# Kernel optimization log

Hardware: AMD Instinct MI355X
Metric: run time of the kernel (lower is better)

The kernel has to match this reference:

```python
import jax, jax.numpy as jnp
import numpy as np

D_MODEL = 1024
N_HEADS = 16
D_HEAD = D_MODEL // N_HEADS
B, T = 2, 2048
EPS = 1e-5


def setup_inputs() -> dict:
    key = jax.random.key(0)
    ks = jax.random.split(key, 5)
    s = 1.0 / np.sqrt(D_MODEL)
    return {
        "x": jax.random.normal(ks[0], (B, T, D_MODEL), dtype=jnp.float32),
        "W_q": jax.random.normal(ks[1], (D_MODEL, D_MODEL), dtype=jnp.float32) * s,
        "W_k": jax.random.normal(ks[2], (D_MODEL, D_MODEL), dtype=jnp.float32) * s,
        "W_v": jax.random.normal(ks[3], (D_MODEL, D_MODEL), dtype=jnp.float32) * s,
        "W_o": jax.random.normal(ks[4], (D_MODEL, D_MODEL), dtype=jnp.float32) * s,
        "gn_weight": jnp.ones((D_MODEL,), dtype=jnp.float32),
        "gn_bias": jnp.zeros((D_MODEL,), dtype=jnp.float32),
    }


def reference(x, W_q, W_k, W_v, W_o, gn_weight, gn_bias):
    b, t, dm = x.shape
    h, dh = N_HEADS, D_HEAD
    # per-head decay factors gamma_i = 1 - 2^(-5-i)
    gammas = 1.0 - 2.0 ** (-5.0 - jnp.arange(h, dtype=jnp.float32))  # [H]

    # projections (torch Linear: y = x @ W.T), split heads -> [B,T,H,Dh]
    q = (x @ W_q.T).reshape(b, t, h, dh)
    k = (x @ W_k.T).reshape(b, t, h, dh)
    v = (x @ W_v.T).reshape(b, t, h, dh)

    # causal decay mask D[h,i,j] = gamma_h^(i-j) for i>=j else 0
    idx = jnp.arange(t)
    diff = idx[:, None] - idx[None, :]                      # [T,T]
    pow_ = jnp.maximum(diff, 0).astype(jnp.float32)
    decay = jnp.where(diff >= 0, gammas[:, None, None] ** pow_, 0.0)  # [H,T,T]

    scale = jnp.sqrt(jnp.float32(dh))
    attn = jnp.einsum('bihd,bjhd->bhij', q, k) * decay[None] / scale  # [B,H,T,T]
    y = jnp.einsum('bhij,bjhd->bihd', attn, v)               # [B,T,H,Dh]

    # GroupNorm(n_heads, d_model) over channels-first layout: per (b, head)
    # normalize over (T, d_head)
    mean = y.mean(axis=(1, 3), keepdims=True)
    var = y.var(axis=(1, 3), keepdims=True)
    yn = (y - mean) / jnp.sqrt(var + EPS)
    yn = yn.reshape(b, t, dm) * gn_weight + gn_bias

    return yn @ W_o.T
```

## Files before the change

kernel.cpp:

```cpp
#include <hip/hip_runtime.h>
#include <stdint.h>


#define SEQ 2048

typedef __bf16 bf16x8 __attribute__((ext_vector_type(8)));
typedef float  floatx4 __attribute__((ext_vector_type(4)));
typedef unsigned short ushort4v __attribute__((ext_vector_type(4)));

__device__ __forceinline__ unsigned short f2bf(float f){
    __bf16 h = (__bf16)f;
    return __builtin_bit_cast(unsigned short, h);
}

__device__ __forceinline__ void gload_lds16(const void* g, void* l){
    __builtin_amdgcn_global_load_lds(
        (const __attribute__((address_space(1))) unsigned int*)g,
        (__attribute__((address_space(3))) unsigned int*)l, 16, 0, 0);
}

__global__ __launch_bounds__(256)
void cvt_all(const float* __restrict__ x,
             const float* __restrict__ w0, const float* __restrict__ w1,
             const float* __restrict__ w2, const float* __restrict__ w3,
             unsigned short* __restrict__ xb,
             unsigned short* __restrict__ o0, unsigned short* __restrict__ o1,
             unsigned short* __restrict__ o2, unsigned short* __restrict__ o3,
             float* __restrict__ st){
    const int blk = blockIdx.x;
    if(blk == 0 && threadIdx.x < 128) st[threadIdx.x] = 0.0f;
    const float* src; unsigned short* dst; size_t i;
    if(blk < 4096){ src = x; dst = xb; i = (size_t)blk*256 + threadIdx.x; }
    else {
        const int seg = (blk - 4096) >> 10;
        src = seg==0?w0:seg==1?w1:seg==2?w2:w3;
        dst = seg==0?o0:seg==1?o1:seg==2?o2:o3;
        i = (size_t)((blk - 4096) & 1023)*256 + threadIdx.x;
    }
    float4 v = ((const float4*)src)[i];
    ushort4v o;
    o[0]=f2bf(v.x); o[1]=f2bf(v.y); o[2]=f2bf(v.z); o[3]=f2bf(v.w);
    *(ushort4v*)&dst[i*4] = o;
}

__global__ __launch_bounds__(256, 3)
void gemm_qkv(const unsigned short* __restrict__ A,
              const unsigned short* __restrict__ Wq,
              const unsigned short* __restrict__ Wk,
              const unsigned short* __restrict__ Wv,
              unsigned short* __restrict__ Qo,
              unsigned short* __restrict__ Ko,
              unsigned short* __restrict__ Vo)
{
    __shared__ unsigned short smem[16384];
    unsigned short* As = smem;
    unsigned short* Bs = smem + 4096;
    const int tid  = threadIdx.x;
    const int w    = tid >> 6, lane = tid & 63, q = lane >> 4, cl = lane & 15;
    const int i0   = blockIdx.x * 128;
    const int ysel = blockIdx.y;
    int mode, n0;
    const unsigned short* Bw;
    unsigned short* O;
    if(ysel < 8)      { mode = 0; Bw = Wq; O = Qo; n0 = ysel*128; }
    else if(ysel < 16){ mode = 1; Bw = Wk; O = Ko; n0 = (ysel-8)*128; }
    else              { mode = 2; Bw = Wv; O = Vo; n0 = (ysel-16)*128; }
    const int wm = (w & 1) * 64, wn = (w >> 1) * 64;

    floatx4 acc[4][4];
    #pragma unroll
    for(int a=0;a<4;a++)
        #pragma unroll
        for(int b=0;b<4;b++) acc[a][b] = (floatx4)(0.0f);

    const int srow = lane >> 2;
    const int soff = (lane & 3) * 16;

    for(int k0 = 0; k0 < 1024; k0 += 32){
        __syncthreads();
        #pragma unroll
        for(int t=0;t<2;t++){
            const int ra = (w*2 + t) * 16;
            gload_lds16((const char*)A  + ((size_t)(i0 + ra + srow)*1024 + k0)*2 + soff,
                        (char*)&As[ra*32]);
            gload_lds16((const char*)Bw + ((size_t)(n0 + ra + srow)*1024 + k0)*2 + soff,
                        (char*)&Bs[ra*32]);
        }
        __syncthreads();

        bf16x8 af[4], bfr[4];
        #pragma unroll
        for(int mi=0;mi<4;mi++) af[mi]  = *(const bf16x8*)&As[(wm + mi*16 + cl)*32 + q*8];
        #pragma unroll
        for(int ni=0;ni<4;ni++) bfr[ni] = *(const bf16x8*)&Bs[(wn + ni*16 + cl)*32 + q*8];
        #pragma unroll
        for(int mi=0;mi<4;mi++)
            #pragma unroll
            for(int ni=0;ni<4;ni++)
                acc[mi][ni] = __builtin_amdgcn_mfma_f32_16x16x32_bf16(af[mi], bfr[ni], acc[mi][ni], 0, 0, 0);
    }

    const int b = i0 >> 11;
    const int tb = i0 & 2047;
    __syncthreads();

    if(mode < 2){
        const int h = (n0 + wn) >> 6;
        const float gamma = 1.0f - __builtin_ldexpf(1.0f, -5 - h);
        const float lgh = log2f(gamma);
        float g1p, base;
        if(mode == 0){ g1p = gamma;        base = exp2f((float)tb * lgh) * 0.125f; }
        else         { g1p = 1.0f / gamma; base = exp2f(-(float)tb * lgh); }
        const float g2 = g1p*g1p, g4 = g2*g2, g8 = g4*g4, g16 = g8*g8;
        const float g32 = g16*g16, g64 = g32*g32;
        float sq = base;
        if(q & 1) sq *= g4;
        if(q & 2) sq *= g8;
        if(wm)    sq *= g64;

        #pragma unroll
        for(int ni=0;ni<4;ni++){
            const int d = wn + ni*16 + cl, d8 = d >> 3, d7 = d & 7;
            float cur = sq;
            #pragma unroll
            for(int mi=0;mi<4;mi++){
                const int tr0 = wm + mi*16 + q*4;
                float v0 = cur, v1 = v0*g1p, v2 = v1*g1p, v3 = v2*g1p;
                smem[(tr0+0)*128 + ((d8 ^ ((tr0+0)&7))*8) + d7] = f2bf(acc[mi][ni][0]*v0);
                smem[(tr0+1)*128 + ((d8 ^ ((tr0+1)&7))*8) + d7] = f2bf(acc[mi][ni][1]*v1);
                smem[(tr0+2)*128 + ((d8 ^ ((tr0+2)&7))*8) + d7] = f2bf(acc[mi][ni][2]*v2);
                smem[(tr0+3)*128 + ((d8 ^ ((tr0+3)&7))*8) + d7] = f2bf(acc[mi][ni][3]*v3);
                cur *= g16;
            }
        }
        __syncthreads();
        const int part = tid & 3;
        #pragma unroll
        for(int rr=0;rr<2;rr++){
            const int row = (tid>>2)*2 + rr;
            const int tt = tb + row;
            #pragma unroll
            for(int k=0;k<4;k++){
                const int c = k*4 + part;
                bf16x8 vrow = *(const bf16x8*)&smem[row*128 + ((c ^ (row&7))*8)];
                const int h2 = (n0 + c*8) >> 6, dd = (c*8) & 63;
                *(bf16x8*)&O[(((size_t)(b*16 + h2))*2048 + tt)*64 + dd] = vrow;
            }
        }
    } else {
        #pragma unroll
        for(int ni=0;ni<4;ni++){
            const int drow = wn + ni*16 + cl, dr7 = drow & 7;
            #pragma unroll
            for(int mi=0;mi<4;mi++){
                const int ch = (wm>>3) + mi*2 + (q>>1);
                const int phys = (ch & 8) | ((ch & 7) ^ dr7);
                ushort4v pk;
                #pragma unroll
                for(int r=0;r<4;r++) pk[r] = f2bf(acc[mi][ni][r]);
                *(ushort4v*)&smem[drow*128 + phys*8 + (q&1)*4] = pk;
            }
        }
        __syncthreads();
        const int part = tid & 3;
        #pragma unroll
        for(int rr=0;rr<2;rr++){
            const int row = (tid>>2)*2 + rr;
            const int dg = n0 + row;
            const int h2 = dg >> 6, dd = dg & 63;
            #pragma unroll
            for(int k=0;k<4;k++){
                const int c = k*4 + part;
                const int phys = (c & 8) | ((c & 7) ^ (row & 7));
                bf16x8 vrow = *(const bf16x8*)&smem[row*128 + phys*8];
                *(bf16x8*)&O[(((size_t)(b*16 + h2))*64 + dd)*2048 + tb + c*8] = vrow;
            }
        }
    }
}

__global__ __launch_bounds__(256, 2)
void retention(const unsigned short* __restrict__ Q,
               const unsigned short* __restrict__ K,
               const unsigned short* __restrict__ VT,
               float* __restrict__ Y0, float* __restrict__ Y1)
{
    __shared__ unsigned short Ks[64*64];
    __shared__ unsigned short Vs[64*64];
    __shared__ unsigned short Ss[4][32*64];

    const int tid = threadIdx.x;
    const int w = tid >> 6, lane = tid & 63, q = lane >> 4, cl = lane & 15;
    const int s = blockIdx.x >> 3, x = blockIdx.x & 7;
    const int bh = blockIdx.y;
    const int wm = w * 32;
    const int l3 = lane >> 3, l7 = lane & 7;
    const int c8 = l7 ^ l3;
    const int cl7 = cl & 7;

    int segbt[2], segjb[2], segje[2], nseg;
    if(s == 0){ nseg = 2;
        segbt[0] = x;     segjb[0] = 0;      segje[0] = 2*x + 2;
        segbt[1] = 15-x;  segjb[1] = 0;      segje[1] = 15 - 2*x;
    } else { nseg = 1;
        segbt[0] = 15-x;  segjb[0] = 15-2*x; segje[0] = 32 - 2*x;
    }

    for(int seg = 0; seg < nseg; seg++){
        const int bt = segbt[seg], jb = segjb[seg], je = segje[seg];
        const int i0 = bt * 128;

        bf16x8 qf[2][2];
        #pragma unroll
        for(int mi=0;mi<2;mi++)
            #pragma unroll
            for(int kk=0;kk<2;kk++)
                qf[mi][kk] = *(const bf16x8*)(Q + ((size_t)bh*SEQ + i0 + wm + mi*16 + cl)*64 + kk*32 + q*8);

        floatx4 Yacc[2][4];
        #pragma unroll
        for(int a=0;a<2;a++)
            #pragma unroll
            for(int b=0;b<4;b++) Yacc[a][b] = (floatx4)(0.0f);

        for(int jt = jb; jt < je; jt++){
            const int j0 = jt * 64;
            __syncthreads();
            #pragma unroll
            for(int t=0;t<2;t++){
                const int r = w*16 + t*8 + l3;
                gload_lds16((const char*)K  + (((size_t)bh*SEQ + j0 + r)*64 + c8*8)*2,
                            (char*)&Ks[(w*16 + t*8)*64]);
                gload_lds16((const char*)VT + (((size_t)bh*64 + r)*SEQ + j0 + c8*8)*2,
                            (char*)&Vs[(w*16 + t*8)*64]);
            }
            __syncthreads();

            floatx4 St[2][4];
            #pragma unroll
            for(int a=0;a<2;a++)
                #pragma unroll
                for(int b=0;b<4;b++) St[a][b] = (floatx4)(0.0f);
            #pragma unroll
            for(int kk=0;kk<2;kk++){
                #pragma unroll
                for(int ni=0;ni<4;ni++){
                    bf16x8 ak = *(const bf16x8*)&Ks[(ni*16 + cl)*64 + ((kk*4+q) ^ cl7)*8];
                    St[0][ni] = __builtin_amdgcn_mfma_f32_16x16x32_bf16(ak, qf[0][kk], St[0][ni], 0,0,0);
                    St[1][ni] = __builtin_amdgcn_mfma_f32_16x16x32_bf16(ak, qf[1][kk], St[1][ni], 0,0,0);
                }
            }

            const bool need_mask = (jt >= 2*bt);
            unsigned short* SsW = Ss[w];
            #pragma unroll
            for(int mi=0;mi<2;mi++){
                const int row = mi*16 + cl;
                const int sw = row & 7;
                const int ig = i0 + wm + row;
                #pragma unroll
                for(int ni=0;ni<4;ni++){
                    ushort4v pk;
                    #pragma unroll
                    for(int r=0;r<4;r++){
                        float v = St[mi][ni][r];
                        if(need_mask){
                            const int jg = j0 + ni*16 + q*4 + r;
                            if(ig < jg) v = 0.0f;
                        }
                        pk[r] = f2bf(v);
                    }
                    *(ushort4v*)&SsW[row*64 + (((ni*2 + (q>>1)) ^ sw)*8) + (q&1)*4] = pk;
                }
            }
            asm volatile("s_waitcnt lgkmcnt(0)" ::: "memory");

            #pragma unroll
            for(int kk=0;kk<2;kk++){
                const int ch = ((kk*4+q) ^ cl7)*8;
                bf16x8 bs0 = *(const bf16x8*)&SsW[( 0 + cl)*64 + ch];
                bf16x8 bs1 = *(const bf16x8*)&SsW[(16 + cl)*64 + ch];
                #pragma unroll
                for(int nt=0;nt<4;nt++){
                    bf16x8 av = *(const bf16x8*)&Vs[(nt*16 + cl)*64 + ch];
                    Yacc[0][nt] = __builtin_amdgcn_mfma_f32_16x16x32_bf16(av, bs0, Yacc[0][nt], 0,0,0);
                    Yacc[1][nt] = __builtin_amdgcn_mfma_f32_16x16x32_bf16(av, bs1, Yacc[1][nt], 0,0,0);
                }
            }
        }

        #pragma unroll
        for(int mi=0;mi<2;mi++)
            #pragma unroll
            for(int nt=0;nt<4;nt++){
                const int ig = i0 + wm + mi*16 + cl;
                #pragma unroll
                for(int r=0;r<4;r++){
                    const int d = nt*16 + q*4 + r;
                    if(s == 0)
                        Y0[((size_t)bh*64 + d)*2048 + ig] = Yacc[mi][nt][r];
                    else
                        Y1[((size_t)bh*64 + d)*1024 + ig - 1024] = Yacc[mi][nt][r];
                }
            }
    }
}

__global__ __launch_bounds__(256)
void gn_stats(const float* __restrict__ Y0, const float* __restrict__ Y1,
              float* __restrict__ st){
    const int g = blockIdx.x >> 3, s8 = blockIdx.x & 7;
    if(g >= 32) return;
    float s1 = 0.f, s2 = 0.f;
    #pragma unroll
    for(int it=0; it<16; it++){
        const int idx = it*256 + threadIdx.x;
        const int dl = idx >> 9;
        const int t4 = idx & 511;
        const int drow = g*64 + s8*8 + dl;
        float4 v = ((const float4*)Y0)[(size_t)drow*512 + t4];
        if(t4 >= 256){
            float4 u = ((const float4*)Y1)[(size_t)drow*256 + t4 - 256];
            v.x += u.x; v.y += u.y; v.z += u.z; v.w += u.w;
        }
        s1 += v.x + v.y + v.z + v.w;
        s2 += v.x*v.x + v.y*v.y + v.z*v.z + v.w*v.w;
    }
    #pragma unroll
    for(int o=32;o>0;o>>=1){ s1 += __shfl_down(s1,o); s2 += __shfl_down(s2,o); }
    __shared__ float r1[4], r2[4];
    const int w = threadIdx.x >> 6, lane = threadIdx.x & 63;
    if(lane == 0){ r1[w] = s1; r2[w] = s2; }
    __syncthreads();
    if(threadIdx.x == 0){
        atomicAdd(&st[g*2+0], r1[0]+r1[1]+r1[2]+r1[3]);
        atomicAdd(&st[g*2+1], r2[0]+r2[1]+r2[2]+r2[3]);
    }
}

__global__ __launch_bounds__(256)
void gn_norm(const float* __restrict__ Y0, const float* __restrict__ Y1,
             const float* __restrict__ st,
             const float* __restrict__ gw, const float* __restrict__ gb,
             unsigned short* __restrict__ Out){
    __shared__ unsigned short T[64*72];
    const int g = blockIdx.x >> 5;
    if(g >= 32) return;
    const int t0 = (blockIdx.x & 31) * 64;
    const int h = g & 15, b = g >> 4;
    const float mean = st[g*2+0] * (1.0f/131072.0f);
    const float var  = st[g*2+1] * (1.0f/131072.0f) - mean*mean;
    const float inv  = rsqrtf(var + 1e-5f);
    const int tid = threadIdx.x;
    const bool hi = (t0 >= 1024);
    #pragma unroll
    for(int kk=0;kk<4;kk++){
        const int f4 = kk*256 + tid;
        const int d = f4 >> 4;
        const int t4l = f4 & 15;
        float4 v = ((const float4*)Y0)[(size_t)(g*64 + d)*512 + (t0>>2) + t4l];
        if(hi){
            float4 u = ((const float4*)Y1)[(size_t)(g*64 + d)*256 + ((t0-1024)>>2) + t4l];
            v.x += u.x; v.y += u.y; v.z += u.z; v.w += u.w;
        }
        const int c = h*64 + d;
        const float sc = inv * gw[c];
        const float bs = gb[c] - mean*sc;
        const int tl = t4l*4;
        T[(tl+0)*72 + d] = f2bf(v.x*sc + bs);
        T[(tl+1)*72 + d] = f2bf(v.y*sc + bs);
        T[(tl+2)*72 + d] = f2bf(v.z*sc + bs);
        T[(tl+3)*72 + d] = f2bf(v.w*sc + bs);
    }
    __syncthreads();
    #pragma unroll
    for(int it=0; it<2; it++){
        const int idx = it*256 + tid;
        const int tl = idx >> 3, segp = idx & 7;
        bf16x8 vrow = *(const bf16x8*)&T[tl*72 + segp*8];
        *(bf16x8*)&Out[((size_t)(b*2048 + t0 + tl))*1024 + h*64 + segp*8] = vrow;
    }
}

__global__ __launch_bounds__(256, 3)
void gemm_out(const unsigned short* __restrict__ A,
              const unsigned short* __restrict__ Bw,
              float* __restrict__ O)
{
    __shared__ unsigned short As[128*32];
    __shared__ unsigned short Bs[64*32];
    const int tid = threadIdx.x;
    const int w = tid >> 6, lane = tid & 63, q = lane >> 4, cl = lane & 15;
    const int i0 = blockIdx.x * 128, n0 = blockIdx.y * 64;
    const int wm = (w & 1) * 64, wn = (w >> 1) * 32;

    floatx4 acc[4][2];
    #pragma unroll
    for(int a=0;a<4;a++)
        #pragma unroll
        for(int b=0;b<2;b++) acc[a][b] = (floatx4)(0.0f);

    const int srow = lane >> 2;
    const int soff = (lane & 3) * 16;

    for(int k0 = 0; k0 < 1024; k0 += 32){
        __syncthreads();
        #pragma unroll
        for(int t=0;t<2;t++){
            const int ra = w*32 + t*16;
            gload_lds16((const char*)A + ((size_t)(i0 + ra + srow)*1024 + k0)*2 + soff,
                        (char*)&As[ra*32]);
        }
        gload_lds16((const char*)Bw + ((size_t)(n0 + w*16 + srow)*1024 + k0)*2 + soff,
                    (char*)&Bs[(w*16)*32]);
        __syncthreads();

        bf16x8 af[4], bfr[2];
        #pragma unroll
        for(int mi=0;mi<4;mi++) af[mi]  = *(const bf16x8*)&As[(wm + mi*16 + cl)*32 + q*8];
        #pragma unroll
        for(int ni=0;ni<2;ni++) bfr[ni] = *(const bf16x8*)&Bs[(wn + ni*16 + cl)*32 + q*8];
        #pragma unroll
        for(int mi=0;mi<4;mi++)
            #pragma unroll
            for(int ni=0;ni<2;ni++)
                acc[mi][ni] = __builtin_amdgcn_mfma_f32_16x16x32_bf16(af[mi], bfr[ni], acc[mi][ni], 0, 0, 0);
    }

    #pragma unroll
    for(int mi=0;mi<4;mi++)
        #pragma unroll
        for(int ni=0;ni<2;ni++){
            const int gi = i0 + wm + mi*16 + q*4;
            const int gn = n0 + wn + ni*16 + cl;
            #pragma unroll
            for(int r=0;r<4;r++) O[(size_t)(gi + r)*1024 + gn] = acc[mi][ni][r];
        }
}

extern "C" void kernel_launch(void* const* d_in, const int* in_sizes, int n_in,
                              void* d_out, int out_size, void* d_ws, size_t ws_size,
                              hipStream_t stream){
    const float* x  = (const float*)d_in[0];
    const float* Wq = (const float*)d_in[1];
    const float* Wk = (const float*)d_in[2];
    const float* Wv = (const float*)d_in[3];
    const float* Wo = (const float*)d_in[4];
    const float* gw = (const float*)d_in[5];
    const float* gb = (const float*)d_in[6];

    char* ws = (char*)d_ws;
    unsigned short* xb  = (unsigned short*)(ws + ((size_t) 0<<20));
    unsigned short* wqb = (unsigned short*)(ws + ((size_t) 8<<20));
    unsigned short* wkb = (unsigned short*)(ws + ((size_t)10<<20));
    unsigned short* wvb = (unsigned short*)(ws + ((size_t)12<<20));
    unsigned short* wob = (unsigned short*)(ws + ((size_t)14<<20));
    unsigned short* qb  = (unsigned short*)(ws + ((size_t)16<<20));
    unsigned short* kb  = (unsigned short*)(ws + ((size_t)24<<20));
    unsigned short* vtb = (unsigned short*)(ws + ((size_t)32<<20));
    float*          y0  = (float*)         (ws + ((size_t)40<<20));
    unsigned short* ynb = (unsigned short*)(ws + ((size_t)56<<20));
    float*          y1  = (float*)         (ws + ((size_t) 0<<20));
    float*          st  = (float*)         (ws + ((size_t)64<<20));

    cvt_all<<<8192, 256, 0, stream>>>(x, Wq, Wk, Wv, Wo, xb, wqb, wkb, wvb, wob, st);

    gemm_qkv<<<dim3(32,24,1), 256, 0, stream>>>(xb, wqb, wkb, wvb, qb, kb, vtb);

    retention<<<dim3(16,32,1), 256, 0, stream>>>(qb, kb, vtb, y0, y1);

    gn_stats<<<256, 256, 0, stream>>>(y0, y1, st);
    gn_norm<<<1024, 256, 0, stream>>>(y0, y1, st, gw, gb, ynb);

    gemm_out<<<dim3(32,16,1), 256, 0, stream>>>(ynb, wob, (float*)d_out);
}
```

Baseline: 185.1 us.

## Double-buffer K/V tiles in retention kernel with a flattened 17-step loop

Doubles the K and V shared-memory tiles so the next tile's global-to-LDS load is issued right after the barrier, while the current tile's score and value MFMAs run. The old per-segment nested loops become one fixed 17-entry loop that maps each step to a row block and key tile. When the row block changes mid-loop, the accumulator is flushed and Q is reloaded. This removes the second barrier per tile and hides load latency, at the cost of twice the K/V LDS footprint, which may pressure occupancy at two blocks per CU.

```diff
diff --git a/kernel.cpp b/kernel.cpp
--- a/kernel.cpp
+++ b/kernel.cpp
@@ -185,8 +185,8 @@
                const unsigned short* __restrict__ VT,
                float* __restrict__ Y0, float* __restrict__ Y1)
 {
-    __shared__ unsigned short Ks[64*64];
-    __shared__ unsigned short Vs[64*64];
+    __shared__ unsigned short Ks[2][64*64];
+    __shared__ unsigned short Vs[2][64*64];
     __shared__ unsigned short Ss[4][32*64];
 
     const int tid = threadIdx.x;
@@ -198,102 +198,34 @@
     const int c8 = l7 ^ l3;
     const int cl7 = cl & 7;
 
-    int segbt[2], segjb[2], segje[2], nseg;
-    if(s == 0){ nseg = 2;
-        segbt[0] = x;     segjb[0] = 0;      segje[0] = 2*x + 2;
-        segbt[1] = 15-x;  segjb[1] = 0;      segje[1] = 15 - 2*x;
-    } else { nseg = 1;
-        segbt[0] = 15-x;  segjb[0] = 15-2*x; segje[0] = 32 - 2*x;
-    }
-
-    for(int seg = 0; seg < nseg; seg++){
-        const int bt = segbt[seg], jb = segjb[seg], je = segje[seg];
-        const int i0 = bt * 128;
-
-        bf16x8 qf[2][2];
+    bf16x8 qf[2][2];
+    floatx4 Yacc[2][4];
+
+    auto entry = [&](int e, int& bt, int& jloc){
+        if(s == 0){
+            if(e <= 2*x+1){ bt = x;    jloc = e; }
+            else          { bt = 15-x; jloc = e - (2*x+2); }
+        } else            { bt = 15-x; jloc = e + 15 - 2*x; }
+    };
+
+    auto stage = [&](int p, int j0){
+        #pragma unroll
+        for(int t=0;t<2;t++){
+            const int r = w*16 + t*8 + l3;
+            gload_lds16((const char*)K  + (((size_t)bh*SEQ + j0 + r)*64 + c8*8)*2,
+                        (char*)&Ks[p][(w*16 + t*8)*64]);
+            gload_lds16((const char*)VT + (((size_t)bh*64 + r)*SEQ + j0 + c8*8)*2,
+                        (char*)&Vs[p][(w*16 + t*8)*64]);
+        }
+    };
+
+    auto flushf = [&](int bt_f){
+        const int i0f = bt_f*128;
         #pragma unroll
         for(int mi=0;mi<2;mi++)
             #pragma unroll
-            for(int kk=0;kk<2;kk++)
-                qf[mi][kk] = *(const bf16x8*)(Q + ((size_t)bh*SEQ + i0 + wm + mi*16 + cl)*64 + kk*32 + q*8);
-
-        floatx4 Yacc[2][4];
-        #pragma unroll
-        for(int a=0;a<2;a++)
-            #pragma unroll
-            for(int b=0;b<4;b++) Yacc[a][b] = (floatx4)(0.0f);
-
-        for(int jt = jb; jt < je; jt++){
-            const int j0 = jt * 64;
-            __syncthreads();
-            #pragma unroll
-            for(int t=0;t<2;t++){
-                const int r = w*16 + t*8 + l3;
-                gload_lds16((const char*)K  + (((size_t)bh*SEQ + j0 + r)*64 + c8*8)*2,
-                            (char*)&Ks[(w*16 + t*8)*64]);
-                gload_lds16((const char*)VT + (((size_t)bh*64 + r)*SEQ + j0 + c8*8)*2,
-                            (char*)&Vs[(w*16 + t*8)*64]);
-            }
-            __syncthreads();
-
-            floatx4 St[2][4];
-            #pragma unroll
-            for(int a=0;a<2;a++)
-                #pragma unroll
-                for(int b=0;b<4;b++) St[a][b] = (floatx4)(0.0f);
-            #pragma unroll
-            for(int kk=0;kk<2;kk++){
-                #pragma unroll
-                for(int ni=0;ni<4;ni++){
-                    bf16x8 ak = *(const bf16x8*)&Ks[(ni*16 + cl)*64 + ((kk*4+q) ^ cl7)*8];
-                    St[0][ni] = __builtin_amdgcn_mfma_f32_16x16x32_bf16(ak, qf[0][kk], St[0][ni], 0,0,0);
-                    St[1][ni] = __builtin_amdgcn_mfma_f32_16x16x32_bf16(ak, qf[1][kk], St[1][ni], 0,0,0);
-                }
-            }
-
-            const bool need_mask = (jt >= 2*bt);
-            unsigned short* SsW = Ss[w];
-            #pragma unroll
-            for(int mi=0;mi<2;mi++){
-                const int row = mi*16 + cl;
-                const int sw = row & 7;
-                const int ig = i0 + wm + row;
-                #pragma unroll
-                for(int ni=0;ni<4;ni++){
-                    ushort4v pk;
-                    #pragma unroll
-                    for(int r=0;r<4;r++){
-                        float v = St[mi][ni][r];
-                        if(need_mask){
-                            const int jg = j0 + ni*16 + q*4 + r;
-                            if(ig < jg) v = 0.0f;
-                        }
-                        pk[r] = f2bf(v);
-                    }
-                    *(ushort4v*)&SsW[row*64 + (((ni*2 + (q>>1)) ^ sw)*8) + (q&1)*4] = pk;
-                }
-            }
-            asm volatile("s_waitcnt lgkmcnt(0)" ::: "memory");
-
-            #pragma unroll
-            for(int kk=0;kk<2;kk++){
-                const int ch = ((kk*4+q) ^ cl7)*8;
-                bf16x8 bs0 = *(const bf16x8*)&SsW[( 0 + cl)*64 + ch];
-                bf16x8 bs1 = *(const bf16x8*)&SsW[(16 + cl)*64 + ch];
-                #pragma unroll
-                for(int nt=0;nt<4;nt++){
-                    bf16x8 av = *(const bf16x8*)&Vs[(nt*16 + cl)*64 + ch];
-                    Yacc[0][nt] = __builtin_amdgcn_mfma_f32_16x16x32_bf16(av, bs0, Yacc[0][nt], 0,0,0);
-                    Yacc[1][nt] = __builtin_amdgcn_mfma_f32_16x16x32_bf16(av, bs1, Yacc[1][nt], 0,0,0);
-                }
-            }
-        }
-
-        #pragma unroll
-        for(int mi=0;mi<2;mi++)
-            #pragma unroll
             for(int nt=0;nt<4;nt++){
-                const int ig = i0 + wm + mi*16 + cl;
+                const int ig = i0f + wm + mi*16 + cl;
                 #pragma unroll
                 for(int r=0;r<4;r++){
                     const int d = nt*16 + q*4 + r;
@@ -303,7 +235,93 @@
                         Y1[((size_t)bh*64 + d)*1024 + ig - 1024] = Yacc[mi][nt][r];
                 }
             }
-    }
+    };
+
+    {
+        int bt0, jl0; entry(0, bt0, jl0);
+        stage(0, jl0*64);
+    }
+
+    int cur_bt = -1;
+    int p = 0;
+    for(int e = 0; e < 17; e++){
+        int bt, jloc; entry(e, bt, jloc);
+        const int i0 = bt*128, j0 = jloc*64;
+
+        if(bt != cur_bt){
+            if(cur_bt >= 0) flushf(cur_bt);
+            #pragma unroll
+            for(int mi=0;mi<2;mi++)
+                #pragma unroll
+                for(int kk=0;kk<2;kk++)
+                    qf[mi][kk] = *(const bf16x8*)(Q + ((size_t)bh*SEQ + i0 + wm + mi*16 + cl)*64 + kk*32 + q*8);
+            #pragma unroll
+            for(int a=0;a<2;a++)
+                #pragma unroll
+                for(int b=0;b<4;b++) Yacc[a][b] = (floatx4)(0.0f);
+            cur_bt = bt;
+        }
+
+        __syncthreads();
+        if(e < 16){ int btn, jln; entry(e+1, btn, jln); stage(p^1, jln*64); }
+
+        const unsigned short* KsP = Ks[p];
+        const unsigned short* VsP = Vs[p];
+
+        floatx4 St[2][4];
+        #pragma unroll
+        for(int a=0;a<2;a++)
+            #pragma unroll
+            for(int b=0;b<4;b++) St[a][b] = (floatx4)(0.0f);
+        #pragma unroll
+        for(int kk=0;kk<2;kk++){
+            #pragma unroll
+            for(int ni=0;ni<4;ni++){
+                bf16x8 ak = *(const bf16x8*)&KsP[(ni*16 + cl)*64 + ((kk*4+q) ^ cl7)*8];
+                St[0][ni] = __builtin_amdgcn_mfma_f32_16x16x32_bf16(ak, qf[0][kk], St[0][ni], 0,0,0);
+                St[1][ni] = __builtin_amdgcn_mfma_f32_16x16x32_bf16(ak, qf[1][kk], St[1][ni], 0,0,0);
+            }
+        }
+
+        const bool need_mask = (jloc >= 2*bt);
+        unsigned short* SsW = Ss[w];
+        #pragma unroll
+        for(int mi=0;mi<2;mi++){
+            const int row = mi*16 + cl;
+            const int sw = row & 7;
+            const int ig = i0 + wm + row;
+            #pragma unroll
+            for(int ni=0;ni<4;ni++){
+                ushort4v pk;
+                #pragma unroll
+                for(int r=0;r<4;r++){
+                    float v = St[mi][ni][r];
+                    if(need_mask){
+                        const int jg = j0 + ni*16 + q*4 + r;
+                        if(ig < jg) v = 0.0f;
+                    }
+                    pk[r] = f2bf(v);
+                }
+                *(ushort4v*)&SsW[row*64 + (((ni*2 + (q>>1)) ^ sw)*8) + (q&1)*4] = pk;
+            }
+        }
+        asm volatile("s_waitcnt lgkmcnt(0)" ::: "memory");
+
+        #pragma unroll
+        for(int kk=0;kk<2;kk++){
+            const int ch = ((kk*4+q) ^ cl7)*8;
+            bf16x8 bs0 = *(const bf16x8*)&SsW[( 0 + cl)*64 + ch];
+            bf16x8 bs1 = *(const bf16x8*)&SsW[(16 + cl)*64 + ch];
+            #pragma unroll
+            for(int nt=0;nt<4;nt++){
+                bf16x8 av = *(const bf16x8*)&VsP[(nt*16 + cl)*64 + ch];
+                Yacc[0][nt] = __builtin_amdgcn_mfma_f32_16x16x32_bf16(av, bs0, Yacc[0][nt], 0,0,0);
+                Yacc[1][nt] = __builtin_amdgcn_mfma_f32_16x16x32_bf16(av, bs1, Yacc[1][nt], 0,0,0);
+            }
+        }
+        p ^= 1;
+    }
+    flushf(cur_bt);
 }
 
 __global__ __launch_bounds__(256)
```

After: 186.5 us. Within noise of the previous version (+0.7%).
